# Performance work log

Hardware: AMD Instinct MI355X
Metric: run time of the kernel (lower is better)

## Reference

```python
import jax, jax.numpy as jnp
import numpy as np

N = 100000       # nodes
E = 1600000      # edges (avg degree 16)
F_IN = 128       # feats_per_node
F1 = 128         # layer_1_feats
F2 = 128         # layer_2_feats


def setup_inputs() -> dict:
    key = jax.random.key(0)
    k1, k2, k3, k4, k5, k6 = jax.random.split(key, 6)
    node_feats = jax.random.normal(k1, (N, F_IN), dtype=jnp.float32)
    # COO representation of sparse normalized adjacency Ahat
    edge_rows = jax.random.randint(k2, (E,), 0, N)
    edge_cols = jax.random.randint(k3, (E,), 0, N)
    edge_vals = jax.random.uniform(k4, (E,), dtype=jnp.float32)
    # reset_param-style init: uniform in +-1/sqrt(fan_in)
    w0 = jax.random.uniform(k5, (F_IN, F1), dtype=jnp.float32,
                            minval=-1.0, maxval=1.0) / np.sqrt(F_IN)
    w1 = jax.random.uniform(k6, (F1, F2), dtype=jnp.float32,
                            minval=-1.0, maxval=1.0) / np.sqrt(F1)
    return {"node_feats": node_feats, "edge_vals": edge_vals,
            "w0": w0, "w1": w1,
            "edge_rows": edge_rows, "edge_cols": edge_cols}


def _spmm(edge_rows, edge_cols, edge_vals, x):
    # out[i] = sum_{(i,j) in edges} val_ij * x[j]   (Ahat @ x)
    msgs = edge_vals[:, None] * x[edge_cols]          # [E, F] gather
    return jax.ops.segment_sum(msgs, edge_rows, num_segments=N)


def reference(node_feats, edge_vals, w0, w1, edge_rows, edge_cols):
    # layer 0: relu(Ahat @ (X @ W0))
    h = jax.nn.relu(_spmm(edge_rows, edge_cols, edge_vals, node_feats @ w0))
    # layer 1: relu(Ahat @ (H @ W1))
    h = jax.nn.relu(_spmm(edge_rows, edge_cols, edge_vals, h @ w1))
    return h
```

## Files before the change

### kernel.cpp

```cpp
#include <hip/hip_runtime.h>

#define N_NODES 100000
#define N_EDGES 1600000
#define F 128
#define M_PAD 100032

#define BUCKET_BITS 9
#define BUCKET_SIZE 512
#define NBUCKETS ((N_NODES + BUCKET_SIZE - 1) / BUCKET_SIZE)
#define EPB_A 8192
#define ABLOCKS ((N_EDGES + EPB_A - 1) / EPB_A)

#define AS1 __attribute__((address_space(1)))
#define AS3 __attribute__((address_space(3)))

typedef __attribute__((ext_vector_type(8))) short short8;
typedef __attribute__((ext_vector_type(4))) float f32x4;

__device__ __forceinline__ float bf_lo(unsigned int u) { return __uint_as_float(u << 16); }
__device__ __forceinline__ float bf_hi(unsigned int u) { return __uint_as_float(u & 0xffff0000u); }
__device__ __forceinline__ unsigned short f2bf(float f) {
    unsigned int u = __float_as_uint(f);
    u += 0x7fffu + ((u >> 16) & 1u);
    return (unsigned short)(u >> 16);
}
__device__ __forceinline__ void gload_lds16(const void* g, void* l) {
    __builtin_amdgcn_global_load_lds((const AS1 unsigned int*)g, (AS3 unsigned int*)l, 16, 0, 0);
}


__global__ __launch_bounds__(256) void bhist_kernel(const int* __restrict__ rows,
                                                    int* __restrict__ ghist) {
    __shared__ int hist[NBUCKETS];
    int tid = threadIdx.x;
    int start = blockIdx.x * EPB_A;
    int cnt = min(EPB_A, N_EDGES - start);
    for (int i = tid; i < NBUCKETS; i += 256) hist[i] = 0;
    __syncthreads();
    for (int i = tid; i < cnt; i += 256) atomicAdd(&hist[rows[start + i] >> BUCKET_BITS], 1);
    __syncthreads();
    for (int i = tid; i < NBUCKETS; i += 256)
        if (hist[i]) atomicAdd(&ghist[i], hist[i]);
}

__global__ __launch_bounds__(256) void bscan_kernel(const int* __restrict__ ghist,
                                                    int* __restrict__ bucket_start,
                                                    int* __restrict__ bucket_cursor) {
    __shared__ int s[256];
    int t = threadIdx.x;
    int v = (t < NBUCKETS) ? ghist[t] : 0;
    s[t] = v;
    __syncthreads();
    for (int off = 1; off < 256; off <<= 1) {
        int x = (t >= off) ? s[t - off] : 0;
        __syncthreads();
        s[t] += x;
        __syncthreads();
    }
    if (t < NBUCKETS) {
        int ex = s[t] - v;
        bucket_start[t] = ex;
        bucket_cursor[t] = ex;
    }
    if (t == NBUCKETS - 1) bucket_start[NBUCKETS] = s[t];
}

__global__ __launch_bounds__(256) void binA_kernel(const int* __restrict__ rows,
                                                   const int* __restrict__ cols,
                                                   const float* __restrict__ vals,
                                                   int* __restrict__ bucket_cursor,
                                                   uint2* __restrict__ stage) {
    __shared__ int hist[NBUCKETS];
    __shared__ int base[NBUCKETS];
    int tid = threadIdx.x;
    int start = blockIdx.x * EPB_A;
    int cnt = min(EPB_A, N_EDGES - start);
    for (int i = tid; i < NBUCKETS; i += 256) hist[i] = 0;
    __syncthreads();
    for (int i = tid; i < cnt; i += 256) atomicAdd(&hist[rows[start + i] >> BUCKET_BITS], 1);
    __syncthreads();
    for (int i = tid; i < NBUCKETS; i += 256) {
        int h = hist[i];
        base[i] = h ? atomicAdd(&bucket_cursor[i], h) : 0;
        hist[i] = 0;
    }
    __syncthreads();
    for (int i = tid; i < cnt; i += 256) {
        int r = rows[start + i];
        int c = cols[start + i];
        unsigned vb = __float_as_uint(vals[start + i]);
        int b = r >> BUCKET_BITS;
        int p = base[b] + atomicAdd(&hist[b], 1);
        stage[p] = make_uint2(((unsigned)(r & (BUCKET_SIZE - 1)) << 17) | (unsigned)c, vb);
    }
}

__global__ __launch_bounds__(1024) void binB_kernel(const uint2* __restrict__ stage,
                                                    const int* __restrict__ bucket_start,
                                                    uint2* __restrict__ csr,
                                                    int* __restrict__ row_start) {
    __shared__ int hist[BUCKET_SIZE];
    __shared__ int scanv[BUCKET_SIZE];
    __shared__ int cur[BUCKET_SIZE];
    int b = blockIdx.x;
    int t = threadIdx.x;
    int s0 = bucket_start[b];
    int cnt = bucket_start[b + 1] - s0;
    if (t < BUCKET_SIZE) hist[t] = 0;
    __syncthreads();
    for (int i = t; i < cnt; i += 1024) atomicAdd(&hist[stage[s0 + i].x >> 17], 1);
    __syncthreads();
    if (t < BUCKET_SIZE) scanv[t] = hist[t];
    __syncthreads();
    for (int off = 1; off < BUCKET_SIZE; off <<= 1) {
        int x = 0;
        if (t < BUCKET_SIZE && t >= off) x = scanv[t - off];
        __syncthreads();
        if (t < BUCKET_SIZE) scanv[t] += x;
        __syncthreads();
    }
    if (t < BUCKET_SIZE) {
        int ex = s0 + scanv[t] - hist[t];
        cur[t] = ex;
        int row = (b << BUCKET_BITS) + t;
        if (row < N_NODES) row_start[row] = ex;
    }
    if (b == 0 && t == 0) row_start[N_NODES] = N_EDGES;
    __syncthreads();
    for (int i = t; i < cnt; i += 1024) {
        uint2 e = stage[s0 + i];
        int p = atomicAdd(&cur[e.x >> 17], 1);
        csr[p] = make_uint2(e.x & 0x1FFFFu, e.y);
    }
}

__global__ __launch_bounds__(256) void wtrans_kernel(const float* __restrict__ W,
                                                     unsigned short* __restrict__ Wt) {
    int t = threadIdx.x;
    int c = t & 127;
    int o0 = (t >> 7) * 8;
    for (int o = o0; o < o0 + 8; ++o) {
        short8 v;
#pragma unroll
        for (int e = 0; e < 8; ++e) v[e] = (short)f2bf(W[(o * 8 + e) * 128 + c]);
        *(short8*)((char*)Wt + c * 256 + ((o * 16) ^ ((c & 7) << 4))) = v;
    }
}

template <bool IN_BF16>
__global__ __launch_bounds__(256) void mfma_gemm_kernel(const void* __restrict__ Av,
                                                        const unsigned short* __restrict__ Wt,
                                                        unsigned short* __restrict__ T) {
    __shared__ alignas(16) unsigned short wlds[128 * 128];
    __shared__ alignas(16) unsigned short alds[64 * 128];
    int tid = threadIdx.x;
    int w = tid >> 6, l = tid & 63;
    int q = l >> 4, c16 = l & 15;
    long r0 = (long)blockIdx.x * 64;

#pragma unroll
    for (int i = 0; i < 8; ++i) {
        int row = w * 32 + i * 4 + q;
        gload_lds16((const char*)Wt + row * 256 + c16 * 16,
                    (char*)wlds + (w * 8192 + i * 1024));
    }
    if constexpr (IN_BF16) {
#pragma unroll
        for (int i = 0; i < 4; ++i) {
            int row = w * 16 + i * 4 + q;
            gload_lds16((const char*)Av + (r0 + row) * 256 + c16 * 16,
                        (char*)alds + (w * 4096 + i * 1024));
        }
    } else {
        const float* X = (const float*)Av;
#pragma unroll
        for (int i = 0; i < 4; ++i) {
            int row = i * 16 + (tid >> 4);
            int oct = tid & 15;
            long rg = r0 + row;
            if (rg > N_NODES - 1) rg = N_NODES - 1;
            const float4* xp = (const float4*)(X + rg * 128 + oct * 8);
            float4 a = xp[0], b = xp[1];
            short8 v;
            v[0] = (short)f2bf(a.x); v[1] = (short)f2bf(a.y);
            v[2] = (short)f2bf(a.z); v[3] = (short)f2bf(a.w);
            v[4] = (short)f2bf(b.x); v[5] = (short)f2bf(b.y);
            v[6] = (short)f2bf(b.z); v[7] = (short)f2bf(b.w);
            *(short8*)((char*)alds + row * 256 + ((oct * 16) ^ ((row & 7) << 4))) = v;
        }
    }
    __syncthreads();

    f32x4 acc[8] = {};
    int nrow = w * 16 + c16;
    int nswz = (nrow & 7) << 4;
#pragma unroll
    for (int ks = 0; ks < 4; ++ks) {
        int kb = ks * 64 + q * 16;
        short8 bfrag = *(const short8*)((const char*)alds + nrow * 256 + (kb ^ nswz));
#pragma unroll
        for (int fb = 0; fb < 8; ++fb) {
            int frow = fb * 16 + c16;
            short8 afrag = *(const short8*)((const char*)wlds + frow * 256 +
                                            (kb ^ ((frow & 7) << 4)));
            acc[fb] = __builtin_amdgcn_mfma_f32_16x16x32_bf16(afrag, bfrag, acc[fb], 0, 0, 0);
        }
    }

    long node = r0 + w * 16 + c16;
#pragma unroll
    for (int fb = 0; fb < 8; ++fb) {
        uint2 o;
        o.x = (unsigned)f2bf(acc[fb][0]) | ((unsigned)f2bf(acc[fb][1]) << 16);
        o.y = (unsigned)f2bf(acc[fb][2]) | ((unsigned)f2bf(acc[fb][3]) << 16);
        *(uint2*)((char*)T + node * 256 + fb * 32 + q * 8) = o;
    }
}

template <bool OUT_BF16>
__global__ __launch_bounds__(256) void spmm_relu_kernel(const int* __restrict__ row_start,
                                                        const uint2* __restrict__ csr,
                                                        const unsigned int* __restrict__ Tu,
                                                        void* __restrict__ outv) {
    int wave = threadIdx.x >> 6;
    int lane = threadIdx.x & 63;
    int row = blockIdx.x * 4 + wave;
    int s = row_start[row];
    int e = row_start[row + 1];
    float ax = 0.f, ay = 0.f;
    for (int base = s; base < e; base += 64) {
        int cnt = min(64, e - base);
        int col_l = 0; float val_l = 0.f;
        if (lane < cnt) {
            uint2 ed = csr[base + lane];
            col_l = (int)ed.x;
            val_l = __uint_as_float(ed.y);
        }
        int j = 0;
        for (; j + 4 <= cnt; j += 4) {
            int   c0 = __shfl(col_l, j),     c1 = __shfl(col_l, j + 1);
            int   c2 = __shfl(col_l, j + 2), c3 = __shfl(col_l, j + 3);
            float v0 = __shfl(val_l, j),     v1 = __shfl(val_l, j + 1);
            float v2 = __shfl(val_l, j + 2), v3 = __shfl(val_l, j + 3);
            unsigned int x0 = Tu[c0 * 64 + lane];
            unsigned int x1 = Tu[c1 * 64 + lane];
            unsigned int x2 = Tu[c2 * 64 + lane];
            unsigned int x3 = Tu[c3 * 64 + lane];
            ax = fmaf(v0, bf_lo(x0), ax); ay = fmaf(v0, bf_hi(x0), ay);
            ax = fmaf(v1, bf_lo(x1), ax); ay = fmaf(v1, bf_hi(x1), ay);
            ax = fmaf(v2, bf_lo(x2), ax); ay = fmaf(v2, bf_hi(x2), ay);
            ax = fmaf(v3, bf_lo(x3), ax); ay = fmaf(v3, bf_hi(x3), ay);
        }
        for (; j < cnt; ++j) {
            int   c = __shfl(col_l, j);
            float v = __shfl(val_l, j);
            unsigned int x = Tu[c * 64 + lane];
            ax = fmaf(v, bf_lo(x), ax); ay = fmaf(v, bf_hi(x), ay);
        }
    }
    ax = fmaxf(ax, 0.f);
    ay = fmaxf(ay, 0.f);
    if constexpr (OUT_BF16) {
        unsigned int* o = (unsigned int*)outv;
        o[row * 64 + (lane ^ ((row & 7) << 2))] =
            (unsigned int)f2bf(ax) | ((unsigned int)f2bf(ay) << 16);
    } else {
        float2* o = (float2*)((float*)outv + row * 128 + lane * 2);
        *o = make_float2(ax, ay);
    }
}

extern "C" void kernel_launch(void* const* d_in, const int* in_sizes, int n_in,
                              void* d_out, int out_size, void* d_ws, size_t ws_size,
                              hipStream_t stream) {
    const float* X     = (const float*)d_in[0];
    const float* evals = (const float*)d_in[1];
    const float* W0    = (const float*)d_in[2];
    const float* W1    = (const float*)d_in[3];
    const int* erows   = (const int*)d_in[4];
    const int* ecols   = (const int*)d_in[5];
    float* out = (float*)d_out;

    char* ws = (char*)d_ws;
    size_t off = 0;
    auto carve = [&](size_t bytes) {
        char* p = ws + off;
        off += (bytes + 255) & ~(size_t)255;
        return p;
    };
    unsigned short* T   = (unsigned short*)carve((size_t)M_PAD * F * 2);
    unsigned short* H   = (unsigned short*)carve((size_t)M_PAD * F * 2);
    unsigned short* Wt0 = (unsigned short*)carve(128 * 128 * 2);
    unsigned short* Wt1 = (unsigned short*)carve(128 * 128 * 2);
    uint2* stage        = (uint2*)carve((size_t)N_EDGES * 8);
    uint2* csr          = (uint2*)carve((size_t)N_EDGES * 8);
    int* row_start      = (int*)carve((size_t)(N_NODES + 1) * 4);
    int* ghist          = (int*)carve((size_t)(NBUCKETS + 1) * 4);
    int* bucket_start   = (int*)carve((size_t)(NBUCKETS + 1) * 4);
    int* bucket_cursor  = (int*)carve((size_t)(NBUCKETS + 1) * 4);
    (void)ws_size; (void)in_sizes; (void)n_in; (void)out_size;

    wtrans_kernel<<<1, 256, 0, stream>>>(W0, Wt0);
    wtrans_kernel<<<1, 256, 0, stream>>>(W1, Wt1);

    hipMemsetAsync(ghist, 0, (size_t)(NBUCKETS + 1) * 4, stream);
    bhist_kernel<<<ABLOCKS, 256, 0, stream>>>(erows, ghist);
    bscan_kernel<<<1, 256, 0, stream>>>(ghist, bucket_start, bucket_cursor);
    binA_kernel<<<ABLOCKS, 256, 0, stream>>>(erows, ecols, evals, bucket_cursor, stage);
    binB_kernel<<<NBUCKETS, 1024, 0, stream>>>(stage, bucket_start, csr, row_start);

    int gemm_grid = M_PAD / 64;

    mfma_gemm_kernel<false><<<gemm_grid, 256, 0, stream>>>(X, Wt0, T);
    spmm_relu_kernel<true><<<N_NODES / 4, 256, 0, stream>>>(row_start, csr,
                                                            (const unsigned int*)T, H);

    mfma_gemm_kernel<true><<<gemm_grid, 256, 0, stream>>>(H, Wt1, T);
    spmm_relu_kernel<false><<<N_NODES / 4, 256, 0, stream>>>(row_start, csr,
                                                             (const unsigned int*)T, out);
}
```

Baseline: 220.5 us.

## Chunk CSR by column range and process 24 rows per wave in SpMM

Replaces the histogram-and-scan bucket sizing with fixed-capacity buckets (BCAP slots each), dropping the bhist and bscan kernels. Within each row the edges are sorted into 7 column chunks, and the SpMM is rewritten so each wave handles 24 interleaved rows and walks them chunk by chunk. Eight rows' gathers are issued together to raise memory-level parallelism and to keep the gathered source rows within a smaller L2-resident window. The cost is heavy register use for 24 accumulator pairs and lockstep padding up to the longest row. The fixed capacity also risks overflowing a bucket if the row distribution is skewed.

```diff
diff --git a/kernel.cpp b/kernel.cpp
--- a/kernel.cpp
+++ b/kernel.cpp
@@ -7,9 +7,18 @@
 
 #define BUCKET_BITS 9
 #define BUCKET_SIZE 512
-#define NBUCKETS ((N_NODES + BUCKET_SIZE - 1) / BUCKET_SIZE)
+#define NBUCKETS 196
+#define BCAP 9216
+#define CHUNK_SHIFT 14
+#define NCHUNK 7
+#define SLOTS (NCHUNK * BUCKET_SIZE)
+#define RS_STRIDE (SLOTS + 1)
 #define EPB_A 8192
-#define ABLOCKS ((N_EDGES + EPB_A - 1) / EPB_A)
+#define ABLOCKS 196
+
+#define SP_BLOCKS 1042
+#define SP_WAVES 4168
+#define ROWS_PW 24
 
 #define AS1 __attribute__((address_space(1)))
 #define AS3 __attribute__((address_space(3)))
@@ -29,40 +38,9 @@
 }
 
 
-__global__ __launch_bounds__(256) void bhist_kernel(const int* __restrict__ rows,
-                                                    int* __restrict__ ghist) {
-    __shared__ int hist[NBUCKETS];
-    int tid = threadIdx.x;
-    int start = blockIdx.x * EPB_A;
-    int cnt = min(EPB_A, N_EDGES - start);
-    for (int i = tid; i < NBUCKETS; i += 256) hist[i] = 0;
-    __syncthreads();
-    for (int i = tid; i < cnt; i += 256) atomicAdd(&hist[rows[start + i] >> BUCKET_BITS], 1);
-    __syncthreads();
-    for (int i = tid; i < NBUCKETS; i += 256)
-        if (hist[i]) atomicAdd(&ghist[i], hist[i]);
-}
-
-__global__ __launch_bounds__(256) void bscan_kernel(const int* __restrict__ ghist,
-                                                    int* __restrict__ bucket_start,
-                                                    int* __restrict__ bucket_cursor) {
-    __shared__ int s[256];
+__global__ void binit_kernel(int* __restrict__ bucket_cursor) {
     int t = threadIdx.x;
-    int v = (t < NBUCKETS) ? ghist[t] : 0;
-    s[t] = v;
-    __syncthreads();
-    for (int off = 1; off < 256; off <<= 1) {
-        int x = (t >= off) ? s[t - off] : 0;
-        __syncthreads();
-        s[t] += x;
-        __syncthreads();
-    }
-    if (t < NBUCKETS) {
-        int ex = s[t] - v;
-        bucket_start[t] = ex;
-        bucket_cursor[t] = ex;
-    }
-    if (t == NBUCKETS - 1) bucket_start[NBUCKETS] = s[t];
+    if (t < NBUCKETS) bucket_cursor[t] = t * BCAP;
 }
 
 __global__ __launch_bounds__(256) void binA_kernel(const int* __restrict__ rows,
@@ -96,41 +74,52 @@
 }
 
 __global__ __launch_bounds__(1024) void binB_kernel(const uint2* __restrict__ stage,
-                                                    const int* __restrict__ bucket_start,
+                                                    const int* __restrict__ bucket_cursor,
                                                     uint2* __restrict__ csr,
-                                                    int* __restrict__ row_start) {
-    __shared__ int hist[BUCKET_SIZE];
-    __shared__ int scanv[BUCKET_SIZE];
-    __shared__ int cur[BUCKET_SIZE];
-    int b = blockIdx.x;
-    int t = threadIdx.x;
-    int s0 = bucket_start[b];
-    int cnt = bucket_start[b + 1] - s0;
-    if (t < BUCKET_SIZE) hist[t] = 0;
-    __syncthreads();
-    for (int i = t; i < cnt; i += 1024) atomicAdd(&hist[stage[s0 + i].x >> 17], 1);
-    __syncthreads();
-    if (t < BUCKET_SIZE) scanv[t] = hist[t];
-    __syncthreads();
-    for (int off = 1; off < BUCKET_SIZE; off <<= 1) {
-        int x = 0;
-        if (t < BUCKET_SIZE && t >= off) x = scanv[t - off];
+                                                    int* __restrict__ rs2) {
+    __shared__ int hist[4096];
+    __shared__ int cur[4096];
+    __shared__ int tsum[1024];
+    int b = blockIdx.x, t = threadIdx.x;
+    int s0 = b * BCAP;
+    int cnt = bucket_cursor[b] - s0;
+#pragma unroll
+    for (int i = 0; i < 4; ++i) hist[t * 4 + i] = 0;
+    __syncthreads();
+    for (int i = t; i < cnt; i += 1024) {
+        unsigned xx = stage[s0 + i].x;
+        int key = ((int)((xx >> CHUNK_SHIFT) & 7u) << BUCKET_BITS) | (int)(xx >> 17);
+        atomicAdd(&hist[key], 1);
+    }
+    __syncthreads();
+    int local = hist[t * 4] + hist[t * 4 + 1] + hist[t * 4 + 2] + hist[t * 4 + 3];
+    tsum[t] = local;
+    __syncthreads();
+    for (int off = 1; off < 1024; off <<= 1) {
+        int xv = (t >= off) ? tsum[t - off] : 0;
         __syncthreads();
-        if (t < BUCKET_SIZE) scanv[t] += x;
+        tsum[t] += xv;
         __syncthreads();
     }
-    if (t < BUCKET_SIZE) {
-        int ex = s0 + scanv[t] - hist[t];
-        cur[t] = ex;
-        int row = (b << BUCKET_BITS) + t;
-        if (row < N_NODES) row_start[row] = ex;
-    }
-    if (b == 0 && t == 0) row_start[N_NODES] = N_EDGES;
+    int running = s0 + tsum[t] - local;
+#pragma unroll
+    for (int i = 0; i < 4; ++i) {
+        int slot = t * 4 + i;
+        if (slot < SLOTS) {
+            cur[slot] = running;
+            rs2[b * RS_STRIDE + slot] = running;
+            running += hist[slot];
+        }
+    }
+    if (t == 1023) rs2[b * RS_STRIDE + SLOTS] = s0 + cnt;
+    for (int p = s0 + cnt + t; p < s0 + BCAP; p += 1024) csr[p] = make_uint2(0u, 0u);
     __syncthreads();
     for (int i = t; i < cnt; i += 1024) {
-        uint2 e = stage[s0 + i];
-        int p = atomicAdd(&cur[e.x >> 17], 1);
-        csr[p] = make_uint2(e.x & 0x1FFFFu, e.y);
+        uint2 ee = stage[s0 + i];
+        unsigned col = ee.x & 0x1FFFFu;
+        int key = ((int)(col >> CHUNK_SHIFT) << BUCKET_BITS) | (int)(ee.x >> 17);
+        int p = atomicAdd(&cur[key], 1);
+        csr[p] = make_uint2(col, ee.y);
     }
 }
 
@@ -180,12 +169,12 @@
             long rg = r0 + row;
             if (rg > N_NODES - 1) rg = N_NODES - 1;
             const float4* xp = (const float4*)(X + rg * 128 + oct * 8);
-            float4 a = xp[0], b = xp[1];
+            float4 a = xp[0], bb = xp[1];
             short8 v;
             v[0] = (short)f2bf(a.x); v[1] = (short)f2bf(a.y);
             v[2] = (short)f2bf(a.z); v[3] = (short)f2bf(a.w);
-            v[4] = (short)f2bf(b.x); v[5] = (short)f2bf(b.y);
-            v[6] = (short)f2bf(b.z); v[7] = (short)f2bf(b.w);
+            v[4] = (short)f2bf(bb.x); v[5] = (short)f2bf(bb.y);
+            v[6] = (short)f2bf(bb.z); v[7] = (short)f2bf(bb.w);
             *(short8*)((char*)alds + row * 256 + ((oct * 16) ^ ((row & 7) << 4))) = v;
         }
     }
@@ -218,55 +207,73 @@
 }
 
 template <bool OUT_BF16>
-__global__ __launch_bounds__(256) void spmm_relu_kernel(const int* __restrict__ row_start,
-                                                        const uint2* __restrict__ csr,
-                                                        const unsigned int* __restrict__ Tu,
-                                                        void* __restrict__ outv) {
-    int wave = threadIdx.x >> 6;
-    int lane = threadIdx.x & 63;
-    int row = blockIdx.x * 4 + wave;
-    int s = row_start[row];
-    int e = row_start[row + 1];
-    float ax = 0.f, ay = 0.f;
-    for (int base = s; base < e; base += 64) {
-        int cnt = min(64, e - base);
-        int col_l = 0; float val_l = 0.f;
-        if (lane < cnt) {
-            uint2 ed = csr[base + lane];
-            col_l = (int)ed.x;
-            val_l = __uint_as_float(ed.y);
-        }
-        int j = 0;
-        for (; j + 4 <= cnt; j += 4) {
-            int   c0 = __shfl(col_l, j),     c1 = __shfl(col_l, j + 1);
-            int   c2 = __shfl(col_l, j + 2), c3 = __shfl(col_l, j + 3);
-            float v0 = __shfl(val_l, j),     v1 = __shfl(val_l, j + 1);
-            float v2 = __shfl(val_l, j + 2), v3 = __shfl(val_l, j + 3);
-            unsigned int x0 = Tu[c0 * 64 + lane];
-            unsigned int x1 = Tu[c1 * 64 + lane];
-            unsigned int x2 = Tu[c2 * 64 + lane];
-            unsigned int x3 = Tu[c3 * 64 + lane];
-            ax = fmaf(v0, bf_lo(x0), ax); ay = fmaf(v0, bf_hi(x0), ay);
-            ax = fmaf(v1, bf_lo(x1), ax); ay = fmaf(v1, bf_hi(x1), ay);
-            ax = fmaf(v2, bf_lo(x2), ax); ay = fmaf(v2, bf_hi(x2), ay);
-            ax = fmaf(v3, bf_lo(x3), ax); ay = fmaf(v3, bf_hi(x3), ay);
-        }
-        for (; j < cnt; ++j) {
-            int   c = __shfl(col_l, j);
-            float v = __shfl(val_l, j);
-            unsigned int x = Tu[c * 64 + lane];
-            ax = fmaf(v, bf_lo(x), ax); ay = fmaf(v, bf_hi(x), ay);
-        }
-    }
-    ax = fmaxf(ax, 0.f);
-    ay = fmaxf(ay, 0.f);
-    if constexpr (OUT_BF16) {
-        unsigned int* o = (unsigned int*)outv;
-        o[row * 64 + (lane ^ ((row & 7) << 2))] =
-            (unsigned int)f2bf(ax) | ((unsigned int)f2bf(ay) << 16);
-    } else {
-        float2* o = (float2*)((float*)outv + row * 128 + lane * 2);
-        *o = make_float2(ax, ay);
+__global__ __launch_bounds__(256, 4) void spmm2_kernel(const int* __restrict__ rs2,
+                                                       const uint2* __restrict__ csr,
+                                                       const unsigned int* __restrict__ Tu,
+                                                       void* __restrict__ outv) {
+    const int wv = blockIdx.x * 4 + (threadIdx.x >> 6);
+    const int lane = threadIdx.x & 63;
+    float ax[ROWS_PW], ay[ROWS_PW];
+#pragma unroll
+    for (int k = 0; k < ROWS_PW; ++k) { ax[k] = 0.f; ay[k] = 0.f; }
+
+    for (int c = 0; c < NCHUNK; ++c) {
+#pragma unroll
+        for (int kg = 0; kg < 3; ++kg) {
+            int s[8], e[8];
+#pragma unroll
+            for (int i = 0; i < 8; ++i) {
+                int row = wv + (kg * 8 + i) * SP_WAVES;
+                int idx = (row >> BUCKET_BITS) * RS_STRIDE + (c << BUCKET_BITS) +
+                          (row & (BUCKET_SIZE - 1));
+                s[i] = rs2[idx];
+                e[i] = rs2[idx + 1];
+            }
+            uint2 ed[8];
+#pragma unroll
+            for (int i = 0; i < 8; ++i) ed[i] = csr[s[i]];
+            unsigned x[8];
+#pragma unroll
+            for (int i = 0; i < 8; ++i) x[i] = Tu[(ed[i].x & 0x1FFFFu) * 64 + lane];
+            int maxlen = 0;
+#pragma unroll
+            for (int i = 0; i < 8; ++i) maxlen = max(maxlen, e[i] - s[i]);
+#pragma unroll
+            for (int i = 0; i < 8; ++i) {
+                float v = (s[i] < e[i]) ? __uint_as_float(ed[i].y) : 0.f;
+                int k = kg * 8 + i;
+                ax[k] = fmaf(v, bf_lo(x[i]), ax[k]);
+                ay[k] = fmaf(v, bf_hi(x[i]), ay[k]);
+            }
+            for (int r = 1; r < maxlen; ++r) {
+                uint2 ed2[8];
+                unsigned x2[8];
+#pragma unroll
+                for (int i = 0; i < 8; ++i) ed2[i] = csr[s[i] + r];
+#pragma unroll
+                for (int i = 0; i < 8; ++i) x2[i] = Tu[(ed2[i].x & 0x1FFFFu) * 64 + lane];
+#pragma unroll
+                for (int i = 0; i < 8; ++i) {
+                    float v = (s[i] + r < e[i]) ? __uint_as_float(ed2[i].y) : 0.f;
+                    int k = kg * 8 + i;
+                    ax[k] = fmaf(v, bf_lo(x2[i]), ax[k]);
+                    ay[k] = fmaf(v, bf_hi(x2[i]), ay[k]);
+                }
+            }
+        }
+    }
+
+#pragma unroll
+    for (int k = 0; k < ROWS_PW; ++k) {
+        int row = wv + k * SP_WAVES;
+        if (k == ROWS_PW - 1 && row >= N_NODES) continue;
+        float vx = fmaxf(ax[k], 0.f), vy = fmaxf(ay[k], 0.f);
+        if constexpr (OUT_BF16) {
+            ((unsigned*)outv)[row * 64 + (lane ^ ((row & 7) << 2))] =
+                (unsigned)f2bf(vx) | ((unsigned)f2bf(vy) << 16);
+        } else {
+            ((float2*)outv)[row * 64 + lane] = make_float2(vx, vy);
+        }
     }
 }
 
@@ -292,30 +299,24 @@
     unsigned short* H   = (unsigned short*)carve((size_t)M_PAD * F * 2);
     unsigned short* Wt0 = (unsigned short*)carve(128 * 128 * 2);
     unsigned short* Wt1 = (unsigned short*)carve(128 * 128 * 2);
-    uint2* stage        = (uint2*)carve((size_t)N_EDGES * 8);
-    uint2* csr          = (uint2*)carve((size_t)N_EDGES * 8);
-    int* row_start      = (int*)carve((size_t)(N_NODES + 1) * 4);
-    int* ghist          = (int*)carve((size_t)(NBUCKETS + 1) * 4);
-    int* bucket_start   = (int*)carve((size_t)(NBUCKETS + 1) * 4);
-    int* bucket_cursor  = (int*)carve((size_t)(NBUCKETS + 1) * 4);
+    uint2* stage        = (uint2*)carve((size_t)NBUCKETS * BCAP * 8);
+    uint2* csr          = (uint2*)carve((size_t)NBUCKETS * BCAP * 8);
+    int* rs2            = (int*)carve(((size_t)NBUCKETS * RS_STRIDE + 1) * 4);
+    int* bucket_cursor  = (int*)carve((size_t)NBUCKETS * 4);
     (void)ws_size; (void)in_sizes; (void)n_in; (void)out_size;
 
     wtrans_kernel<<<1, 256, 0, stream>>>(W0, Wt0);
     wtrans_kernel<<<1, 256, 0, stream>>>(W1, Wt1);
 
-    hipMemsetAsync(ghist, 0, (size_t)(NBUCKETS + 1) * 4, stream);
-    bhist_kernel<<<ABLOCKS, 256, 0, stream>>>(erows, ghist);
-    bscan_kernel<<<1, 256, 0, stream>>>(ghist, bucket_start, bucket_cursor);
+    binit_kernel<<<1, 256, 0, stream>>>(bucket_cursor);
     binA_kernel<<<ABLOCKS, 256, 0, stream>>>(erows, ecols, evals, bucket_cursor, stage);
-    binB_kernel<<<NBUCKETS, 1024, 0, stream>>>(stage, bucket_start, csr, row_start);
+    binB_kernel<<<NBUCKETS, 1024, 0, stream>>>(stage, bucket_cursor, csr, rs2);
 
     int gemm_grid = M_PAD / 64;
 
     mfma_gemm_kernel<false><<<gemm_grid, 256, 0, stream>>>(X, Wt0, T);
-    spmm_relu_kernel<true><<<N_NODES / 4, 256, 0, stream>>>(row_start, csr,
-                                                            (const unsigned int*)T, H);
+    spmm2_kernel<true><<<SP_BLOCKS, 256, 0, stream>>>(rs2, csr, (const unsigned int*)T, H);
 
     mfma_gemm_kernel<true><<<gemm_grid, 256, 0, stream>>>(H, Wt1, T);
-    spmm_relu_kernel<false><<<N_NODES / 4, 256, 0, stream>>>(row_start, csr,
-                                                             (const unsigned int*)T, out);
-}
+    spmm2_kernel<false><<<SP_BLOCKS, 256, 0, stream>>>(rs2, csr, (const unsigned int*)T, out);
+}
```

Result: slower. 572.5 us (+159.6%).

## Use fixed-capacity buckets to drop histogram pass; unroll SpMM gathers by eight

Applied to the files above, without the earlier changes.

Replaces the global bucket histogram and scan with fixed-capacity bucket slots (BCAP per bucket), so binning skips one full pass over the edge rows plus a memset and a scan launch. Row boundaries become per-row (start,end) pairs because bucket segments are no longer contiguous. The SpMM inner loop now issues eight independent gathers before accumulating, which raises memory-level parallelism. The fixed capacity assumes no bucket exceeds 9216 edges, which only holds for the expected random input distribution and risks overflow on skewed graphs.

```diff
diff --git a/kernel.cpp b/kernel.cpp
--- a/kernel.cpp
+++ b/kernel.cpp
@@ -7,9 +7,10 @@
 
 #define BUCKET_BITS 9
 #define BUCKET_SIZE 512
-#define NBUCKETS ((N_NODES + BUCKET_SIZE - 1) / BUCKET_SIZE)
+#define NBUCKETS 196
+#define BCAP 9216
 #define EPB_A 8192
-#define ABLOCKS ((N_EDGES + EPB_A - 1) / EPB_A)
+#define ABLOCKS 196
 
 #define AS1 __attribute__((address_space(1)))
 #define AS3 __attribute__((address_space(3)))
@@ -29,40 +30,9 @@
 }
 
 
-__global__ __launch_bounds__(256) void bhist_kernel(const int* __restrict__ rows,
-                                                    int* __restrict__ ghist) {
-    __shared__ int hist[NBUCKETS];
-    int tid = threadIdx.x;
-    int start = blockIdx.x * EPB_A;
-    int cnt = min(EPB_A, N_EDGES - start);
-    for (int i = tid; i < NBUCKETS; i += 256) hist[i] = 0;
-    __syncthreads();
-    for (int i = tid; i < cnt; i += 256) atomicAdd(&hist[rows[start + i] >> BUCKET_BITS], 1);
-    __syncthreads();
-    for (int i = tid; i < NBUCKETS; i += 256)
-        if (hist[i]) atomicAdd(&ghist[i], hist[i]);
-}
-
-__global__ __launch_bounds__(256) void bscan_kernel(const int* __restrict__ ghist,
-                                                    int* __restrict__ bucket_start,
-                                                    int* __restrict__ bucket_cursor) {
-    __shared__ int s[256];
+__global__ void binit_kernel(int* __restrict__ bucket_cursor) {
     int t = threadIdx.x;
-    int v = (t < NBUCKETS) ? ghist[t] : 0;
-    s[t] = v;
-    __syncthreads();
-    for (int off = 1; off < 256; off <<= 1) {
-        int x = (t >= off) ? s[t - off] : 0;
-        __syncthreads();
-        s[t] += x;
-        __syncthreads();
-    }
-    if (t < NBUCKETS) {
-        int ex = s[t] - v;
-        bucket_start[t] = ex;
-        bucket_cursor[t] = ex;
-    }
-    if (t == NBUCKETS - 1) bucket_start[NBUCKETS] = s[t];
+    if (t < NBUCKETS) bucket_cursor[t] = t * BCAP;
 }
 
 __global__ __launch_bounds__(256) void binA_kernel(const int* __restrict__ rows,
@@ -96,16 +66,16 @@
 }
 
 __global__ __launch_bounds__(1024) void binB_kernel(const uint2* __restrict__ stage,
-                                                    const int* __restrict__ bucket_start,
+                                                    const int* __restrict__ bucket_cursor,
                                                     uint2* __restrict__ csr,
-                                                    int* __restrict__ row_start) {
+                                                    uint2* __restrict__ rowseg) {
     __shared__ int hist[BUCKET_SIZE];
     __shared__ int scanv[BUCKET_SIZE];
     __shared__ int cur[BUCKET_SIZE];
     int b = blockIdx.x;
     int t = threadIdx.x;
-    int s0 = bucket_start[b];
-    int cnt = bucket_start[b + 1] - s0;
+    int s0 = b * BCAP;
+    int cnt = bucket_cursor[b] - s0;
     if (t < BUCKET_SIZE) hist[t] = 0;
     __syncthreads();
     for (int i = t; i < cnt; i += 1024) atomicAdd(&hist[stage[s0 + i].x >> 17], 1);
@@ -120,12 +90,11 @@
         __syncthreads();
     }
     if (t < BUCKET_SIZE) {
-        int ex = s0 + scanv[t] - hist[t];
-        cur[t] = ex;
+        int st = s0 + scanv[t] - hist[t];
+        cur[t] = st;
         int row = (b << BUCKET_BITS) + t;
-        if (row < N_NODES) row_start[row] = ex;
-    }
-    if (b == 0 && t == 0) row_start[N_NODES] = N_EDGES;
+        if (row < N_NODES) rowseg[row] = make_uint2((unsigned)st, (unsigned)(st + hist[t]));
+    }
     __syncthreads();
     for (int i = t; i < cnt; i += 1024) {
         uint2 e = stage[s0 + i];
@@ -180,12 +149,12 @@
             long rg = r0 + row;
             if (rg > N_NODES - 1) rg = N_NODES - 1;
             const float4* xp = (const float4*)(X + rg * 128 + oct * 8);
-            float4 a = xp[0], b = xp[1];
+            float4 a = xp[0], bb = xp[1];
             short8 v;
             v[0] = (short)f2bf(a.x); v[1] = (short)f2bf(a.y);
             v[2] = (short)f2bf(a.z); v[3] = (short)f2bf(a.w);
-            v[4] = (short)f2bf(b.x); v[5] = (short)f2bf(b.y);
-            v[6] = (short)f2bf(b.z); v[7] = (short)f2bf(b.w);
+            v[4] = (short)f2bf(bb.x); v[5] = (short)f2bf(bb.y);
+            v[6] = (short)f2bf(bb.z); v[7] = (short)f2bf(bb.w);
             *(short8*)((char*)alds + row * 256 + ((oct * 16) ^ ((row & 7) << 4))) = v;
         }
     }
@@ -218,15 +187,16 @@
 }
 
 template <bool OUT_BF16>
-__global__ __launch_bounds__(256) void spmm_relu_kernel(const int* __restrict__ row_start,
+__global__ __launch_bounds__(256) void spmm_relu_kernel(const uint2* __restrict__ rowseg,
                                                         const uint2* __restrict__ csr,
                                                         const unsigned int* __restrict__ Tu,
                                                         void* __restrict__ outv) {
     int wave = threadIdx.x >> 6;
     int lane = threadIdx.x & 63;
     int row = blockIdx.x * 4 + wave;
-    int s = row_start[row];
-    int e = row_start[row + 1];
+    uint2 se = rowseg[row];
+    int s = (int)se.x;
+    int e = (int)se.y;
     float ax = 0.f, ay = 0.f;
     for (int base = s; base < e; base += 64) {
         int cnt = min(64, e - base);
@@ -237,24 +207,33 @@
             val_l = __uint_as_float(ed.y);
         }
         int j = 0;
-        for (; j + 4 <= cnt; j += 4) {
+        for (; j + 8 <= cnt; j += 8) {
+            int cc[8]; float vv[8]; unsigned xx[8];
+#pragma unroll
+            for (int i = 0; i < 8; ++i) {
+                cc[i] = __shfl(col_l, j + i);
+                vv[i] = __shfl(val_l, j + i);
+            }
+#pragma unroll
+            for (int i = 0; i < 8; ++i) xx[i] = Tu[cc[i] * 64 + lane];
+#pragma unroll
+            for (int i = 0; i < 8; ++i) {
+                ax = fmaf(vv[i], bf_lo(xx[i]), ax);
+                ay = fmaf(vv[i], bf_hi(xx[i]), ay);
+            }
+        }
+        for (; j + 2 <= cnt; j += 2) {
             int   c0 = __shfl(col_l, j),     c1 = __shfl(col_l, j + 1);
-            int   c2 = __shfl(col_l, j + 2), c3 = __shfl(col_l, j + 3);
             float v0 = __shfl(val_l, j),     v1 = __shfl(val_l, j + 1);
-            float v2 = __shfl(val_l, j + 2), v3 = __shfl(val_l, j + 3);
-            unsigned int x0 = Tu[c0 * 64 + lane];
-            unsigned int x1 = Tu[c1 * 64 + lane];
-            unsigned int x2 = Tu[c2 * 64 + lane];
-            unsigned int x3 = Tu[c3 * 64 + lane];
+            unsigned x0 = Tu[c0 * 64 + lane];
+            unsigned x1 = Tu[c1 * 64 + lane];
             ax = fmaf(v0, bf_lo(x0), ax); ay = fmaf(v0, bf_hi(x0), ay);
             ax = fmaf(v1, bf_lo(x1), ax); ay = fmaf(v1, bf_hi(x1), ay);
-            ax = fmaf(v2, bf_lo(x2), ax); ay = fmaf(v2, bf_hi(x2), ay);
-            ax = fmaf(v3, bf_lo(x3), ax); ay = fmaf(v3, bf_hi(x3), ay);
         }
         for (; j < cnt; ++j) {
             int   c = __shfl(col_l, j);
             float v = __shfl(val_l, j);
-            unsigned int x = Tu[c * 64 + lane];
+            unsigned x = Tu[c * 64 + lane];
             ax = fmaf(v, bf_lo(x), ax); ay = fmaf(v, bf_hi(x), ay);
         }
     }
@@ -292,30 +271,26 @@
     unsigned short* H   = (unsigned short*)carve((size_t)M_PAD * F * 2);
     unsigned short* Wt0 = (unsigned short*)carve(128 * 128 * 2);
     unsigned short* Wt1 = (unsigned short*)carve(128 * 128 * 2);
-    uint2* stage        = (uint2*)carve((size_t)N_EDGES * 8);
-    uint2* csr          = (uint2*)carve((size_t)N_EDGES * 8);
-    int* row_start      = (int*)carve((size_t)(N_NODES + 1) * 4);
-    int* ghist          = (int*)carve((size_t)(NBUCKETS + 1) * 4);
-    int* bucket_start   = (int*)carve((size_t)(NBUCKETS + 1) * 4);
-    int* bucket_cursor  = (int*)carve((size_t)(NBUCKETS + 1) * 4);
+    uint2* stage        = (uint2*)carve((size_t)NBUCKETS * BCAP * 8);
+    uint2* csr          = (uint2*)carve((size_t)NBUCKETS * BCAP * 8);
+    uint2* rowseg       = (uint2*)carve((size_t)N_NODES * 8);
+    int* bucket_cursor  = (int*)carve((size_t)NBUCKETS * 4);
     (void)ws_size; (void)in_sizes; (void)n_in; (void)out_size;
 
     wtrans_kernel<<<1, 256, 0, stream>>>(W0, Wt0);
     wtrans_kernel<<<1, 256, 0, stream>>>(W1, Wt1);
 
-    hipMemsetAsync(ghist, 0, (size_t)(NBUCKETS + 1) * 4, stream);
-    bhist_kernel<<<ABLOCKS, 256, 0, stream>>>(erows, ghist);
-    bscan_kernel<<<1, 256, 0, stream>>>(ghist, bucket_start, bucket_cursor);
+    binit_kernel<<<1, 256, 0, stream>>>(bucket_cursor);
     binA_kernel<<<ABLOCKS, 256, 0, stream>>>(erows, ecols, evals, bucket_cursor, stage);
-    binB_kernel<<<NBUCKETS, 1024, 0, stream>>>(stage, bucket_start, csr, row_start);
+    binB_kernel<<<NBUCKETS, 1024, 0, stream>>>(stage, bucket_cursor, csr, rowseg);
 
     int gemm_grid = M_PAD / 64;
 
     mfma_gemm_kernel<false><<<gemm_grid, 256, 0, stream>>>(X, Wt0, T);
-    spmm_relu_kernel<true><<<N_NODES / 4, 256, 0, stream>>>(row_start, csr,
+    spmm_relu_kernel<true><<<N_NODES / 4, 256, 0, stream>>>(rowseg, csr,
                                                             (const unsigned int*)T, H);
 
     mfma_gemm_kernel<true><<<gemm_grid, 256, 0, stream>>>(H, Wt1, T);
-    spmm_relu_kernel<false><<<N_NODES / 4, 256, 0, stream>>>(row_start, csr,
+    spmm_relu_kernel<false><<<N_NODES / 4, 256, 0, stream>>>(rowseg, csr,
                                                              (const unsigned int*)T, out);
 }
```

New measurement: 202.4 us. 1.09x faster.
